# Performance work log

Measured on AMD Instinct MI355X. Metric: run time of the kernel, lower is better.

## Reference

```python
import jax, jax.numpy as jnp
import numpy as np

B, N, K, C = 16, 1024, 64, 128
TEMPERATURE = 0.07


def _l2_normalize(x, eps=1e-12):
    # matches torch F.normalize(dim=-1): x / max(||x||, eps)
    n = jnp.linalg.norm(x, axis=-1, keepdims=True)
    return x / jnp.maximum(n, eps)


def setup_inputs() -> dict:
    key = jax.random.key(0)
    k1, k2, k3, k4 = jax.random.split(key, 4)
    q = jax.random.normal(k1, (B, N, C), dtype=jnp.float32)
    k = jax.random.normal(k2, (B, N, C), dtype=jnp.float32)
    positive_indices = jax.random.randint(k3, (B, N), 0, N)
    negative_indices = jax.random.randint(k4, (B, N, K), 0, N)
    return {"q": q, "k": k,
            "positive_indices": positive_indices,
            "negative_indices": negative_indices}


def reference(q, k, positive_indices, negative_indices):
    qn = _l2_normalize(q)                                   # (B,N,C)
    kn = _l2_normalize(k)                                   # (B,N,C)

    pos_valid = positive_indices >= 0                       # (B,N)
    pos_idx = jnp.where(pos_valid, positive_indices, 0)
    positive = jnp.take_along_axis(kn, pos_idx[..., None], axis=1)  # (B,N,C)
    pos_sim = jnp.sum(qn * positive, axis=-1) / TEMPERATURE          # (B,N)

    neg_valid = negative_indices >= 0                       # (B,N,K)
    neg_idx = jnp.where(neg_valid, negative_indices, 0)
    # batched ragged gather of negatives: (B,N,K,C)
    negs = jax.vmap(lambda kb, idx: kb[idx])(kn, neg_idx)
    neg_sim = jnp.einsum('bnc,bnkc->bnk', qn, negs) / TEMPERATURE    # (B,N,K)
    neg_sim = jnp.where(neg_valid, neg_sim, -jnp.inf)

    # cross-entropy with label 0 over [pos, negs]:
    # loss = logsumexp(logits) - pos_sim
    logits = jnp.concatenate([pos_sim[..., None], neg_sim], axis=-1)  # (B,N,1+K)
    per_patch = jax.nn.logsumexp(logits, axis=-1) - pos_sim           # (B,N)

    total = jnp.sum(jnp.where(pos_valid, per_patch, 0.0))
    count = jnp.sum(pos_valid)
    return jnp.where(count > 0, total / jnp.maximum(count, 1), 0.0)
```

## Files before the change

### kernel.cpp

```cpp
#include <hip/hip_runtime.h>
#include <math.h>

#define B_ 16
#define N_ 1024
#define K_ 64
#define C_ 128
#define INV_T 14.285714285714286f
#define NBLK_MAIN 1024

__device__ __forceinline__ float waveReduceSum(float v) {
#pragma unroll
    for (int off = 32; off > 0; off >>= 1)
        v += __shfl_xor(v, off, 64);
    return v;
}

__device__ __forceinline__ float waveReduceMax(float v) {
#pragma unroll
    for (int off = 32; off > 0; off >>= 1)
        v = fmaxf(v, __shfl_xor(v, off, 64));
    return v;
}

__global__ __launch_bounds__(256) void infonce_kernel(
    const float* __restrict__ q, const float* __restrict__ k,
    const int* __restrict__ pos_idx, const int* __restrict__ neg_idx,
    float* __restrict__ partials) {
    __shared__ float q_lds[4][C_];
    __shared__ float wave_tot[4], wave_cnt[4];

    const int lane = threadIdx.x & 63;
    const int wid  = threadIdx.x >> 6;
    const int g    = lane >> 3;
    const int s    = lane & 7;

    const int batch = blockIdx.x & 15;
    const int chunk = blockIdx.x >> 4;
    const int rbase = chunk * 16 + wid * 4;

    const float* kb = k + (size_t)batch * (N_ * C_);

    float tot = 0.0f, cnt = 0.0f;

    for (int r = 0; r < 4; ++r) {
        const int n   = rbase + r;
        const int row = batch * N_ + n;

        const float* qrow = q + (size_t)row * C_;
        const float2 qv = *(const float2*)(qrow + 2 * lane);
        *(float2*)(&q_lds[wid][2 * lane]) = qv;

        const int  pidx = pos_idx[row];
        const bool pval = pidx >= 0;
        const int  p0   = pval ? pidx : 0;
        const float2 pk = *(const float2*)(kb + (size_t)p0 * C_ + 2 * lane);
        float qss = qv.x * qv.x + qv.y * qv.y;
        float pd  = qv.x * pk.x + qv.y * pk.y;
        float pss = pk.x * pk.x + pk.y * pk.y;
#pragma unroll
        for (int off = 32; off > 0; off >>= 1) {
            qss += __shfl_xor(qss, off, 64);
            pd  += __shfl_xor(pd,  off, 64);
            pss += __shfl_xor(pss, off, 64);
        }
        const float inv_q   = 1.0f / fmaxf(sqrtf(qss), 1e-12f);
        const float pos_sim = pd * inv_q / fmaxf(sqrtf(pss), 1e-12f) * INV_T;

        const int my_nidx = neg_idx[(size_t)row * K_ + lane];

        __syncthreads();

        float4 q4[4];
#pragma unroll
        for (int i = 0; i < 4; ++i)
            q4[i] = *(const float4*)(&q_lds[wid][i * 32 + s * 4]);

        float simv[8];
#pragma unroll
        for (int p = 0; p < 8; ++p) {
            const int  nidx = __shfl(my_nidx, p * 8 + g, 64);
            const bool nval = nidx >= 0;
            const float* kr = kb + (size_t)(nval ? nidx : 0) * C_;
            float dot = 0.0f, kss = 0.0f;
#pragma unroll
            for (int i = 0; i < 4; ++i) {
                const float4 kv = *(const float4*)(kr + i * 32 + s * 4);
                dot = fmaf(kv.x, q4[i].x, dot);
                dot = fmaf(kv.y, q4[i].y, dot);
                dot = fmaf(kv.z, q4[i].z, dot);
                dot = fmaf(kv.w, q4[i].w, dot);
                kss = fmaf(kv.x, kv.x, kss);
                kss = fmaf(kv.y, kv.y, kss);
                kss = fmaf(kv.z, kv.z, kss);
                kss = fmaf(kv.w, kv.w, kss);
            }
#pragma unroll
            for (int off = 1; off < 8; off <<= 1) {
                dot += __shfl_xor(dot, off, 64);
                kss += __shfl_xor(kss, off, 64);
            }
            simv[p] = nval ? dot * inv_q / fmaxf(sqrtf(kss), 1e-12f) * INV_T
                           : -INFINITY;
        }

        float m = pos_sim;
#pragma unroll
        for (int p = 0; p < 8; ++p) m = fmaxf(m, simv[p]);
        m = waveReduceMax(m);
        float ssum = 0.0f;
        if (s == 0) {
#pragma unroll
            for (int p = 0; p < 8; ++p) ssum += __expf(simv[p] - m);
        }
        ssum = waveReduceSum(ssum) + __expf(pos_sim - m);
        const float per_patch = m + __logf(ssum) - pos_sim;

        if (pval) { tot += per_patch; cnt += 1.0f; }
        __syncthreads();
    }

    if (lane == 0) { wave_tot[wid] = tot; wave_cnt[wid] = cnt; }
    __syncthreads();
    if (threadIdx.x == 0) {
        partials[2 * blockIdx.x]     = wave_tot[0] + wave_tot[1] + wave_tot[2] + wave_tot[3];
        partials[2 * blockIdx.x + 1] = wave_cnt[0] + wave_cnt[1] + wave_cnt[2] + wave_cnt[3];
    }
}

__global__ __launch_bounds__(256) void finalize_kernel(const float* __restrict__ partials,
                                                       float* __restrict__ out, int nblocks) {
    __shared__ float st[256], sc[256];
    float t = 0.0f, c = 0.0f;
    for (int i = threadIdx.x; i < nblocks; i += 256) {
        t += partials[2 * i];
        c += partials[2 * i + 1];
    }
    st[threadIdx.x] = t;
    sc[threadIdx.x] = c;
    __syncthreads();
    for (int off = 128; off > 0; off >>= 1) {
        if (threadIdx.x < off) {
            st[threadIdx.x] += st[threadIdx.x + off];
            sc[threadIdx.x] += sc[threadIdx.x + off];
        }
        __syncthreads();
    }
    if (threadIdx.x == 0) {
        const float cntv = sc[0];
        out[0] = (cntv > 0.0f) ? st[0] / fmaxf(cntv, 1.0f) : 0.0f;
    }
}

extern "C" void kernel_launch(void* const* d_in, const int* in_sizes, int n_in,
                              void* d_out, int out_size, void* d_ws, size_t ws_size,
                              hipStream_t stream) {
    const float* q   = (const float*)d_in[0];
    const float* k   = (const float*)d_in[1];
    const int*   pos = (const int*)d_in[2];
    const int*   neg = (const int*)d_in[3];
    float* out = (float*)d_out;
    float* ws  = (float*)d_ws;

    float* partials = ws;

    infonce_kernel<<<NBLK_MAIN, 256, 0, stream>>>(q, k, pos, neg, partials);
    finalize_kernel<<<1, 256, 0, stream>>>(partials, out, NBLK_MAIN);
}
```

Before: 99.99 us.

## Precompute key inverse norms in separate kernel and fold positive dot into gather loop

Adds a pre-pass kernel that computes 1/||k|| for every key row once, so the main kernel no longer recomputes squared norms for each gathered negative. The positive dot and the q self-dot are handled as a ninth gather slot in the same 8-lane reduction loop, and the __syncthreads calls inside the row loop are removed. Rows per block are halved and the grid doubled, with a launch_bounds occupancy hint. This trades an extra kernel launch and a small workspace buffer for less ALU and shuffle work per negative, relying on wave-local LDS use being safe without barriers.

Measured after the change: 102.1 us. 2.1% more time.

```diff
diff --git a/kernel.cpp b/kernel.cpp
--- a/kernel.cpp
+++ b/kernel.cpp
@@ -6,7 +6,7 @@
 #define K_ 64
 #define C_ 128
 #define INV_T 14.285714285714286f
-#define NBLK_MAIN 1024
+#define NBLK_MAIN 2048
 
 __device__ __forceinline__ float waveReduceSum(float v) {
 #pragma unroll
@@ -22,10 +22,24 @@
     return v;
 }
 
-__global__ __launch_bounds__(256) void infonce_kernel(
+__global__ __launch_bounds__(256) void knorm_kernel(const float* __restrict__ k,
+                                                    float* __restrict__ inv_k) {
+    const int lane = threadIdx.x & 63;
+    const int wid  = threadIdx.x >> 6;
+    const int base = blockIdx.x * 16 + wid * 4;
+#pragma unroll
+    for (int r = 0; r < 4; ++r) {
+        const int row = base + r;
+        const float2 kv = *(const float2*)(k + (size_t)row * C_ + 2 * lane);
+        float ss = waveReduceSum(kv.x * kv.x + kv.y * kv.y);
+        if (lane == 0) inv_k[row] = 1.0f / fmaxf(sqrtf(ss), 1e-12f);
+    }
+}
+
+__global__ __launch_bounds__(256, 4) void infonce_kernel(
     const float* __restrict__ q, const float* __restrict__ k,
     const int* __restrict__ pos_idx, const int* __restrict__ neg_idx,
-    float* __restrict__ partials) {
+    const float* __restrict__ inv_k, float* __restrict__ partials) {
     __shared__ float q_lds[4][C_];
     __shared__ float wave_tot[4], wave_cnt[4];
 
@@ -36,52 +50,44 @@
 
     const int batch = blockIdx.x & 15;
     const int chunk = blockIdx.x >> 4;
-    const int rbase = chunk * 16 + wid * 4;
+    const int rbase = chunk * 8 + wid * 2;
 
-    const float* kb = k + (size_t)batch * (N_ * C_);
+    const float* kb    = k + (size_t)batch * (N_ * C_);
+    const float* invkb = inv_k + batch * N_;
 
     float tot = 0.0f, cnt = 0.0f;
 
-    for (int r = 0; r < 4; ++r) {
+#pragma unroll
+    for (int r = 0; r < 2; ++r) {
         const int n   = rbase + r;
         const int row = batch * N_ + n;
+        const float* qrow = q + (size_t)row * C_;
 
-        const float* qrow = q + (size_t)row * C_;
         const float2 qv = *(const float2*)(qrow + 2 * lane);
         *(float2*)(&q_lds[wid][2 * lane]) = qv;
 
         const int  pidx = pos_idx[row];
         const bool pval = pidx >= 0;
         const int  p0   = pval ? pidx : 0;
-        const float2 pk = *(const float2*)(kb + (size_t)p0 * C_ + 2 * lane);
-        float qss = qv.x * qv.x + qv.y * qv.y;
-        float pd  = qv.x * pk.x + qv.y * pk.y;
-        float pss = pk.x * pk.x + pk.y * pk.y;
-#pragma unroll
-        for (int off = 32; off > 0; off >>= 1) {
-            qss += __shfl_xor(qss, off, 64);
-            pd  += __shfl_xor(pd,  off, 64);
-            pss += __shfl_xor(pss, off, 64);
-        }
-        const float inv_q   = 1.0f / fmaxf(sqrtf(qss), 1e-12f);
-        const float pos_sim = pd * inv_q / fmaxf(sqrtf(pss), 1e-12f) * INV_T;
 
         const int my_nidx = neg_idx[(size_t)row * K_ + lane];
 
-        __syncthreads();
+        int nidx[8];
+#pragma unroll
+        for (int p = 0; p < 8; ++p) nidx[p] = __shfl(my_nidx, p * 8 + g, 64);
 
         float4 q4[4];
 #pragma unroll
         for (int i = 0; i < 4; ++i)
             q4[i] = *(const float4*)(&q_lds[wid][i * 32 + s * 4]);
 
-        float simv[8];
+        float d[9];
 #pragma unroll
-        for (int p = 0; p < 8; ++p) {
-            const int  nidx = __shfl(my_nidx, p * 8 + g, 64);
-            const bool nval = nidx >= 0;
-            const float* kr = kb + (size_t)(nval ? nidx : 0) * C_;
-            float dot = 0.0f, kss = 0.0f;
+        for (int p = 0; p < 9; ++p) {
+            const float* kr;
+            if (p < 8) kr = kb + (size_t)(nidx[p] >= 0 ? nidx[p] : 0) * C_;
+            else       kr = (g == 0) ? (kb + (size_t)p0 * C_) : qrow;
+            float dot = 0.0f;
 #pragma unroll
             for (int i = 0; i < 4; ++i) {
                 const float4 kv = *(const float4*)(kr + i * 32 + s * 4);
@@ -89,18 +95,24 @@
                 dot = fmaf(kv.y, q4[i].y, dot);
                 dot = fmaf(kv.z, q4[i].z, dot);
                 dot = fmaf(kv.w, q4[i].w, dot);
-                kss = fmaf(kv.x, kv.x, kss);
-                kss = fmaf(kv.y, kv.y, kss);
-                kss = fmaf(kv.z, kv.z, kss);
-                kss = fmaf(kv.w, kv.w, kss);
             }
+            dot += __shfl_xor(dot, 1, 64);
+            dot += __shfl_xor(dot, 2, 64);
+            dot += __shfl_xor(dot, 4, 64);
+            d[p] = dot;
+        }
+
+        const float pos_dot = __int_as_float(__builtin_amdgcn_readlane(__float_as_int(d[8]), 0));
+        const float qss     = __int_as_float(__builtin_amdgcn_readlane(__float_as_int(d[8]), 8));
+        const float scale   = (1.0f / fmaxf(sqrtf(qss), 1e-12f)) * INV_T;
+        const float pos_sim = pos_dot * scale * invkb[p0];
+
+        float simv[8];
 #pragma unroll
-            for (int off = 1; off < 8; off <<= 1) {
-                dot += __shfl_xor(dot, off, 64);
-                kss += __shfl_xor(kss, off, 64);
-            }
-            simv[p] = nval ? dot * inv_q / fmaxf(sqrtf(kss), 1e-12f) * INV_T
-                           : -INFINITY;
+        for (int p = 0; p < 8; ++p) {
+            const bool nv = nidx[p] >= 0;
+            const float ik = invkb[nv ? nidx[p] : 0];
+            simv[p] = nv ? d[p] * scale * ik : -INFINITY;
         }
 
         float m = pos_sim;
@@ -116,7 +128,6 @@
         const float per_patch = m + __logf(ssum) - pos_sim;
 
         if (pval) { tot += per_patch; cnt += 1.0f; }
-        __syncthreads();
     }
 
     if (lane == 0) { wave_tot[wid] = tot; wave_cnt[wid] = cnt; }
@@ -162,7 +173,9 @@
     float* ws  = (float*)d_ws;
 
     float* partials = ws;
+    float* inv_k    = ws + 2 * NBLK_MAIN;
 
-    infonce_kernel<<<NBLK_MAIN, 256, 0, stream>>>(q, k, pos, neg, partials);
+    knorm_kernel<<<1024, 256, 0, stream>>>(k, inv_k);
+    infonce_kernel<<<NBLK_MAIN, 256, 0, stream>>>(q, k, pos, neg, inv_k, partials);
     finalize_kernel<<<1, 256, 0, stream>>>(partials, out, NBLK_MAIN);
 }
```
